# Kernel optimization log

Hardware: AMD Instinct MI355X
Metric: run time of the kernel (lower is better)

## Reference

```python
import jax, jax.numpy as jnp
import numpy as np

B, S, D = 2, 2048, 768
H = 12
DH = D // H
EPS = 1e-12


def setup_inputs() -> dict:
    key = jax.random.key(0)
    ks = jax.random.split(key, 16)
    s = 0.02
    return {
        "hidden_states": jax.random.normal(ks[0], (B, S, D), jnp.float32),
        "attention_mask": jnp.zeros((B, 1, 1, S), jnp.float32),
        "position_bias": jax.random.normal(ks[1], (1, H, S, S), jnp.float32),
        "q_w": jax.random.normal(ks[2], (D, D), jnp.float32) * s,
        "q_b": jnp.zeros((D,), jnp.float32),
        "k_w": jax.random.normal(ks[3], (D, D), jnp.float32) * s,
        "k_b": jnp.zeros((D,), jnp.float32),
        "v_w": jax.random.normal(ks[4], (D, D), jnp.float32) * s,
        "v_b": jnp.zeros((D,), jnp.float32),
        "o_w": jax.random.normal(ks[5], (D, D), jnp.float32) * s,
        "o_b": jnp.zeros((D,), jnp.float32),
        "ln_w": jnp.ones((D,), jnp.float32),
        "ln_b": jnp.zeros((D,), jnp.float32),
    }


def _split_heads(x):
    # [B, S, D] -> [B, H, S, DH]
    b, s, _ = x.shape
    return x.reshape(b, s, H, DH).transpose(0, 2, 1, 3)


def reference(hidden_states, attention_mask, position_bias,
              q_w, q_b, k_w, k_b, v_w, v_b, o_w, o_b, ln_w, ln_b):
    # nn.Linear: y = x @ W.T + b (W stored [out, in])
    q = _split_heads(hidden_states @ q_w.T + q_b)
    k = _split_heads(hidden_states @ k_w.T + k_b)
    v = _split_heads(hidden_states @ v_w.T + v_b)

    scale = 1.0 / jnp.sqrt(jnp.asarray(DH, hidden_states.dtype))
    scores = jnp.einsum('bhqd,bhkd->bhqk', q, k) * scale
    scores = scores + position_bias + attention_mask
    probs = jax.nn.softmax(scores, axis=-1)

    c = jnp.einsum('bhqk,bhkd->bhqd', probs, v)
    c = c.transpose(0, 2, 1, 3).reshape(hidden_states.shape[0], -1, D)
    o = c @ o_w.T + o_b

    # residual + LayerNorm (dropout is identity at eval)
    x = o + hidden_states
    mu = jnp.mean(x, axis=-1, keepdims=True)
    var = jnp.mean(jnp.square(x - mu), axis=-1, keepdims=True)
    out = (x - mu) * jax.lax.rsqrt(var + EPS) * ln_w + ln_b
    return out
```

## Files before the change

### kernel.cpp

```cpp
#include <hip/hip_runtime.h>
#include <math.h>

typedef unsigned short u16;
typedef float f32x4 __attribute__((ext_vector_type(4)));
typedef __bf16 bf16x8 __attribute__((ext_vector_type(8)));

#define B_ 2
#define S_ 2048
#define D_ 768
#define H_ 12
#define DH_ 64

__device__ __forceinline__ u16 f2bf(float x) {
  union { float f; unsigned u; } v; v.f = x;
  unsigned r = v.u + 0x7fffu + ((v.u >> 16) & 1u);
  return (u16)(r >> 16);
}

__device__ __forceinline__ f32x4 zero4() { f32x4 z = {0.f, 0.f, 0.f, 0.f}; return z; }

__device__ __forceinline__ f32x4 mfma16(bf16x8 a, bf16x8 b, f32x4 c) {
  return __builtin_amdgcn_mfma_f32_16x16x32_bf16(a, b, c, 0, 0, 0);
}

__device__ __forceinline__ void gload_lds16(const void* g, void* l) {
  __builtin_amdgcn_global_load_lds((const __attribute__((address_space(1))) void*)g,
                                   (__attribute__((address_space(3))) void*)l, 16, 0, 0);
}

__global__ void cvt_kernel(const float* __restrict__ hid, const float* __restrict__ qw,
                           const float* __restrict__ kw, const float* __restrict__ vw,
                           const float* __restrict__ ow, u16* __restrict__ Hb,
                           u16* __restrict__ Wb) {
  const int NH = B_ * S_ * D_;
  const int NW = D_ * D_;
  const int T4 = (NH + 4 * NW) >> 2;
  int stride = gridDim.x * blockDim.x;
  for (int i = blockIdx.x * blockDim.x + threadIdx.x; i < T4; i += stride) {
    int e = i << 2;
    const float* src; u16* dst;
    if (e < NH) { src = hid + e; dst = Hb + e; }
    else {
      int o = e - NH;
      int m = o / NW, oo = o - m * NW;
      src = (m == 0 ? qw : m == 1 ? kw : m == 2 ? vw : ow) + oo;
      dst = Wb + o;
    }
    f32x4 v = *(const f32x4*)src;
    uint2 o2;
    o2.x = (unsigned)f2bf(v[0]) | ((unsigned)f2bf(v[1]) << 16);
    o2.y = (unsigned)f2bf(v[2]) | ((unsigned)f2bf(v[3]) << 16);
    *(uint2*)dst = o2;
  }
}

#define BM 128
#define BN 128
#define BK 64

__global__ __launch_bounds__(256) void gemm_kernel(
    const u16* __restrict__ A, const u16* __restrict__ W,
    const float* __restrict__ bq, const float* __restrict__ bk, const float* __restrict__ bv,
    u16* __restrict__ Qb, u16* __restrict__ Kb, u16* __restrict__ Vtmp,
    float* __restrict__ Of, const float* __restrict__ bO, int mode)
{
  __shared__ __align__(16) u16 As[BM * BK];
  __shared__ __align__(16) u16 Bs[BN * BK];
  int t = threadIdx.x;
  int lane = t & 63, w = t >> 6;
  int wr = w >> 1, wc = w & 1;
  int l15 = lane & 15, l4 = lane >> 4;
  int m0 = blockIdx.y * BM, n0 = blockIdx.x * BN;

  f32x4 acc[4][4];
#pragma unroll
  for (int i = 0; i < 4; ++i)
#pragma unroll
    for (int j = 0; j < 4; ++j) acc[i][j] = zero4();

  const int K = D_;
  for (int k0 = 0; k0 < K; k0 += BK) {
    __syncthreads();
#pragma unroll
    for (int p = 0; p < 4; ++p) {
      int seg = p * 4 + w;
      int bd = seg * 64 + lane;
      int row = bd >> 3;
      int slot = (bd & 7) ^ (row & 7);
      gload_lds16(A + (size_t)(m0 + row) * K + k0 + slot * 8, (char*)As + seg * 1024);
      gload_lds16(W + (size_t)(n0 + row) * K + k0 + slot * 8, (char*)Bs + seg * 1024);
    }
    __syncthreads();
#pragma unroll
    for (int kk = 0; kk < 2; ++kk) {
      bf16x8 af[4], bfr[4];
#pragma unroll
      for (int i = 0; i < 4; ++i) {
        int ra = wr * 64 + i * 16 + l15;
        af[i] = *(const bf16x8*)((const char*)As + ra * 128 +
                                 ((kk * 64 + (l4 << 4)) ^ ((ra & 7) << 4)));
        int rb = wc * 64 + i * 16 + l15;
        bfr[i] = *(const bf16x8*)((const char*)Bs + rb * 128 +
                                  ((kk * 64 + (l4 << 4)) ^ ((rb & 7) << 4)));
      }
#pragma unroll
      for (int i = 0; i < 4; ++i)
#pragma unroll
        for (int j = 0; j < 4; ++j)
          acc[i][j] = mfma16(af[i], bfr[j], acc[i][j]);
    }
  }

  if (mode == 0) {
    int mat = n0 / D_;
    int ncol0 = (n0 - mat * D_) + wc * 64;
    const float* bias = (mat == 0) ? bq : (mat == 1 ? bk : bv);
    u16* outp = (mat == 0) ? Qb : (mat == 1 ? Kb : Vtmp);
    float scale = (mat == 0) ? 0.125f : 1.0f;
    int h = ncol0 >> 6;
#pragma unroll
    for (int j = 0; j < 4; ++j) {
      int d = j * 16 + l15;
      float bvv = bias[ncol0 + d];
#pragma unroll
      for (int i = 0; i < 4; ++i) {
#pragma unroll
        for (int r = 0; r < 4; ++r) {
          int m = m0 + wr * 64 + i * 16 + (l4 << 2) + r;
          int bb = m >> 11, ss = m & 2047;
          float val = (acc[i][j][r] + bvv) * scale;
          outp[(((size_t)bb * H_ + h) * S_ + ss) * DH_ + d] = f2bf(val);
        }
      }
    }
  } else {
#pragma unroll
    for (int j = 0; j < 4; ++j) {
      int n = n0 + wc * 64 + j * 16 + l15;
      float bvv = bO[n];
#pragma unroll
      for (int i = 0; i < 4; ++i) {
#pragma unroll
        for (int r = 0; r < 4; ++r) {
          int m = m0 + wr * 64 + i * 16 + (l4 << 2) + r;
          Of[(size_t)m * D_ + n] = acc[i][j][r] + bvv;
        }
      }
    }
  }
}

__global__ __launch_bounds__(256) void vtrans_kernel(const u16* __restrict__ V,
                                                     u16* __restrict__ Vt) {
  __shared__ __align__(16) u16 tile[64 * 64];
  int t = threadIdx.x;
  int s0 = blockIdx.x * 64;
  int bh = blockIdx.y;
  const u16* src = V + ((size_t)bh * S_ + s0) * DH_;
#pragma unroll
  for (int p = 0; p < 2; ++p) {
    int bd = t + p * 256;
    int row = bd >> 3, slot = bd & 7;
    uint4 v = *(const uint4*)(src + row * 64 + slot * 8);
    *(uint4*)((char*)tile + row * 128 + ((slot ^ (row & 7)) << 4)) = v;
  }
  __syncthreads();
  int d = t >> 2, sc = (t & 3) * 16;
  u16* dst = Vt + ((size_t)bh * DH_ + d) * S_ + s0 + sc;
  int colB = d * 2;
#pragma unroll
  for (int half = 0; half < 2; ++half) {
    u16 tmp[8] __attribute__((aligned(16)));
#pragma unroll
    for (int j = 0; j < 8; ++j) {
      int s = sc + half * 8 + j;
      tmp[j] = *(const u16*)((const char*)tile + s * 128 +
                             (((colB >> 4) ^ (s & 7)) << 4) + (colB & 15));
    }
    *(uint4*)(dst + half * 8) = *(const uint4*)tmp;
  }
}

__global__ __launch_bounds__(512, 6) void attn_kernel(
    const u16* __restrict__ Qb, const u16* __restrict__ Kb, const u16* __restrict__ Vt,
    const float* __restrict__ bias, const float* __restrict__ mask, u16* __restrict__ Cb)
{
  __shared__ __align__(16) u16 Ks[2][64 * 64];
  __shared__ __align__(16) u16 Vs[2][64 * 64];
  __shared__ __align__(16) char upool[17408];
  u16 (*Ps)[16][72] = (u16 (*)[16][72])upool;
  float (*Osh)[16][66] = (float (*)[16][66])upool;
  float (*Lsh)[2][16] = (float (*)[2][16])(upool + 16896);

  int t = threadIdx.x, lane = t & 63, w = t >> 6;
  int qg = w & 3, kg = w >> 2;
  int q0 = blockIdx.x * 64, h = blockIdx.y, b = blockIdx.z;
  size_t bh = (size_t)b * H_ + h;
  const u16* Qp = Qb + (bh * S_ + q0) * DH_;
  const u16* Kp = Kb + bh * S_ * DH_;
  const u16* Vp = Vt + bh * DH_ * S_;
  const float* biasp = bias + ((size_t)h * S_ + q0) * S_;
  const float* maskp = mask + (size_t)b * S_;
  int l15 = lane & 15, l4 = lane >> 4;
  int kc0 = kg * 32;

  const float* brp0 = biasp + (size_t)(qg * 16 + (l4 << 2) + 0) * S_ + kc0 + l15;
  const float* brp1 = brp0 + S_;
  const float* brp2 = brp1 + S_;
  const float* brp3 = brp2 + S_;
  const float* mkp = maskp + kc0 + l15;

  bf16x8 qf0, qf1;
  {
    const u16* qrow = Qp + (qg * 16 + l15) * DH_;
    qf0 = *(const bf16x8*)(qrow + l4 * 8);
    qf1 = *(const bf16x8*)(qrow + 32 + l4 * 8);
  }

  f32x4 oacc[4];
#pragma unroll
  for (int i = 0; i < 4; ++i) oacc[i] = zero4();
  float lrow[4] = {0.f, 0.f, 0.f, 0.f};

  float bc0[2], bc1[2], bc2[2], bc3[2];
  float bn0[2], bn1[2], bn2[2], bn3[2];

  {
    int row = t >> 3;
    int slot = (t & 7) ^ (row & 7);
    gload_lds16(Kp + (size_t)row * DH_ + slot * 8, (char*)Ks[0] + w * 1024);
    gload_lds16(Vp + (size_t)row * S_ + slot * 8, (char*)Vs[0] + w * 1024);
  }
#pragma unroll
  for (int kf = 0; kf < 2; ++kf) {
    float mk = mkp[kf * 16];
    bc0[kf] = brp0[kf * 16] + mk;
    bc1[kf] = brp1[kf * 16] + mk;
    bc2[kf] = brp2[kf * 16] + mk;
    bc3[kf] = brp3[kf * 16] + mk;
  }
  __syncthreads();

  int cur = 0;
  for (int kt = 0; kt < S_ / 64; ++kt) {
    int k0 = kt * 64;
    if (kt + 1 < S_ / 64) {
      int k0n = k0 + 64;
      int row = t >> 3;
      int slot = (t & 7) ^ (row & 7);
      gload_lds16(Kp + (size_t)(k0n + row) * DH_ + slot * 8, (char*)Ks[cur ^ 1] + w * 1024);
      gload_lds16(Vp + (size_t)row * S_ + k0n + slot * 8, (char*)Vs[cur ^ 1] + w * 1024);
#pragma unroll
      for (int kf = 0; kf < 2; ++kf) {
        float mk = mkp[k0n + kf * 16];
        bn0[kf] = brp0[k0n + kf * 16] + mk;
        bn1[kf] = brp1[k0n + kf * 16] + mk;
        bn2[kf] = brp2[k0n + kf * 16] + mk;
        bn3[kf] = brp3[k0n + kf * 16] + mk;
      }
    }

    const u16* Kc = Ks[cur];
    const u16* Vc = Vs[cur];

    f32x4 sf[2];
#pragma unroll
    for (int kf = 0; kf < 2; ++kf) {
      int row = kc0 + kf * 16 + l15;
      bf16x8 kb0 = *(const bf16x8*)((const char*)Kc + row * 128 +
                                    ((l4 << 4) ^ ((row & 7) << 4)));
      bf16x8 kb1 = *(const bf16x8*)((const char*)Kc + row * 128 +
                                    ((64 + (l4 << 4)) ^ ((row & 7) << 4)));
      f32x4 s0 = zero4();
      s0 = mfma16(qf0, kb0, s0);
      s0 = mfma16(qf1, kb1, s0);
      sf[kf] = s0;
    }

#pragma unroll
    for (int kf = 0; kf < 2; ++kf) {
      float p0 = __expf(sf[kf][0] + bc0[kf]);
      float p1 = __expf(sf[kf][1] + bc1[kf]);
      float p2 = __expf(sf[kf][2] + bc2[kf]);
      float p3 = __expf(sf[kf][3] + bc3[kf]);
      sf[kf][0] = p0; sf[kf][1] = p1; sf[kf][2] = p2; sf[kf][3] = p3;
      lrow[0] += p0; lrow[1] += p1; lrow[2] += p2; lrow[3] += p3;
    }

#pragma unroll
    for (int r = 0; r < 4; ++r)
#pragma unroll
      for (int kf = 0; kf < 2; ++kf)
        Ps[qg][(l4 << 2) + r][kc0 + kf * 16 + l15] = f2bf(sf[kf][r]);

    bf16x8 pa = *(const bf16x8*)&Ps[qg][l15][kc0 + l4 * 8];

#pragma unroll
    for (int df = 0; df < 4; ++df) {
      int row = df * 16 + l15;
      bf16x8 vb = *(const bf16x8*)((const char*)Vc + row * 128 +
                                   ((kg * 64 + (l4 << 4)) ^ ((row & 7) << 4)));
      oacc[df] = mfma16(pa, vb, oacc[df]);
    }

    __syncthreads();
    cur ^= 1;
#pragma unroll
    for (int kf = 0; kf < 2; ++kf) {
      bc0[kf] = bn0[kf]; bc1[kf] = bn1[kf];
      bc2[kf] = bn2[kf]; bc3[kf] = bn3[kf];
    }
  }

#pragma unroll
  for (int r = 0; r < 4; ++r) {
#pragma unroll
    for (int o = 1; o < 16; o <<= 1) lrow[r] += __shfl_xor(lrow[r], o, 64);
  }
  if (l15 == 0) {
#pragma unroll
    for (int r = 0; r < 4; ++r) Lsh[qg][kg][(l4 << 2) + r] = lrow[r];
  }
  if (kg == 1) {
#pragma unroll
    for (int r = 0; r < 4; ++r)
#pragma unroll
      for (int df = 0; df < 4; ++df)
        Osh[qg][(l4 << 2) + r][df * 16 + l15] = oacc[df][r];
  }
  __syncthreads();
  if (kg == 0) {
#pragma unroll
    for (int r = 0; r < 4; ++r) {
      int rr = (l4 << 2) + r;
      float inv = 1.0f / (Lsh[qg][0][rr] + Lsh[qg][1][rr]);
      int q = q0 + qg * 16 + rr;
      size_t base = ((size_t)b * S_ + q) * D_ + h * DH_ + l15;
#pragma unroll
      for (int df = 0; df < 4; ++df)
        Cb[base + df * 16] = f2bf((oacc[df][r] + Osh[qg][rr][df * 16 + l15]) * inv);
    }
  }
}

__global__ __launch_bounds__(192) void ln_kernel(const float* __restrict__ O,
                                                 const float* __restrict__ hid,
                                                 const float* __restrict__ lw,
                                                 const float* __restrict__ lb,
                                                 float* __restrict__ out) {
  int row = blockIdx.x, t = threadIdx.x;
  size_t base = (size_t)row * D_;
  f32x4 x = *(const f32x4*)(O + base + t * 4);
  f32x4 hh = *(const f32x4*)(hid + base + t * 4);
  x = x + hh;
  float s = x[0] + x[1] + x[2] + x[3];
  float s2 = x[0] * x[0] + x[1] * x[1] + x[2] * x[2] + x[3] * x[3];
#pragma unroll
  for (int o = 1; o < 64; o <<= 1) {
    s += __shfl_xor(s, o, 64);
    s2 += __shfl_xor(s2, o, 64);
  }
  __shared__ float rs[3], rs2[3];
  int w = t >> 6, lane = t & 63;
  if (lane == 0) { rs[w] = s; rs2[w] = s2; }
  __syncthreads();
  s = rs[0] + rs[1] + rs[2];
  s2 = rs2[0] + rs2[1] + rs2[2];
  float mu = s * (1.0f / 768.0f);
  float var = s2 * (1.0f / 768.0f) - mu * mu;
  float rstd = rsqrtf(var + 1e-12f);
  f32x4 w4 = *(const f32x4*)(lw + t * 4);
  f32x4 b4 = *(const f32x4*)(lb + t * 4);
  f32x4 y = (x - mu) * rstd * w4 + b4;
  *(f32x4*)(out + base + t * 4) = y;
}

extern "C" void kernel_launch(void* const* d_in, const int* in_sizes, int n_in,
                              void* d_out, int out_size, void* d_ws, size_t ws_size,
                              hipStream_t stream) {
  const float* hid  = (const float*)d_in[0];
  const float* mask = (const float*)d_in[1];
  const float* bias = (const float*)d_in[2];
  const float* qw = (const float*)d_in[3];
  const float* qb = (const float*)d_in[4];
  const float* kw = (const float*)d_in[5];
  const float* kb = (const float*)d_in[6];
  const float* vw = (const float*)d_in[7];
  const float* vb = (const float*)d_in[8];
  const float* ow = (const float*)d_in[9];
  const float* ob = (const float*)d_in[10];
  const float* lnw = (const float*)d_in[11];
  const float* lnb = (const float*)d_in[12];

  char* ws = (char*)d_ws;
  const size_t NHB = (size_t)B_ * S_ * D_ * 2;
  const size_t NWB = (size_t)4 * D_ * D_ * 2;
  const size_t NQB = (size_t)B_ * H_ * S_ * DH_ * 2;
  u16* Hb = (u16*)ws;
  u16* Wb = (u16*)(ws + NHB);
  u16* Qb = (u16*)(ws + NHB + NWB);
  u16* Kb = (u16*)(ws + NHB + NWB + NQB);
  u16* Vt = (u16*)(ws + NHB + NWB + 2 * NQB);
  u16* Cb = (u16*)(ws + NHB + NWB + 3 * NQB);
  float* Of = (float*)(ws + NHB + NWB + 4 * NQB);
  u16* Vtmp = (u16*)Of;

  cvt_kernel<<<2048, 256, 0, stream>>>(hid, qw, kw, vw, ow, Hb, Wb);

  gemm_kernel<<<dim3(18, 32), 256, 0, stream>>>(
      Hb, Wb, qb, kb, vb, Qb, Kb, Vtmp, nullptr, nullptr, 0);

  vtrans_kernel<<<dim3(S_ / 64, B_ * H_), 256, 0, stream>>>(Vtmp, Vt);

  attn_kernel<<<dim3(S_ / 64, H_, B_), 512, 0, stream>>>(Qb, Kb, Vt, bias, mask, Cb);

  gemm_kernel<<<dim3(6, 32), 256, 0, stream>>>(
      Cb, Wb + (size_t)3 * D_ * D_, nullptr, nullptr, nullptr,
      nullptr, nullptr, nullptr, Of, ob, 1);

  ln_kernel<<<B_ * S_, 192, 0, stream>>>(Of, hid, lnw, lnb, (float*)d_out);
}
```

Measured before the change: 149.8 us.

## Replace async LDS loads with register-staged two-tile-ahead prefetch pipeline

```diff
diff --git a/kernel.cpp b/kernel.cpp
--- a/kernel.cpp
+++ b/kernel.cpp
@@ -181,7 +181,7 @@
   }
 }
 
-__global__ __launch_bounds__(512, 6) void attn_kernel(
+__global__ __launch_bounds__(512, 4) void attn_kernel(
     const u16* __restrict__ Qb, const u16* __restrict__ Kb, const u16* __restrict__ Vt,
     const float* __restrict__ bias, const float* __restrict__ mask, u16* __restrict__ Cb)
 {
@@ -210,6 +210,11 @@
   const float* brp3 = brp2 + S_;
   const float* mkp = maskp + kc0 + l15;
 
+  int srow = t >> 3, sslot = t & 7;
+  const u16* gK = Kp + (size_t)srow * DH_ + sslot * 8;
+  const u16* gV = Vp + (size_t)srow * S_ + sslot * 8;
+  int lofs = srow * 128 + ((sslot ^ (srow & 7)) << 4);
+
   bf16x8 qf0, qf1;
   {
     const u16* qrow = Qp + (qg * 16 + l15) * DH_;
@@ -222,94 +227,143 @@
   for (int i = 0; i < 4; ++i) oacc[i] = zero4();
   float lrow[4] = {0.f, 0.f, 0.f, 0.f};
 
-  float bc0[2], bc1[2], bc2[2], bc3[2];
-  float bn0[2], bn1[2], bn2[2], bn3[2];
-
-  {
-    int row = t >> 3;
-    int slot = (t & 7) ^ (row & 7);
-    gload_lds16(Kp + (size_t)row * DH_ + slot * 8, (char*)Ks[0] + w * 1024);
-    gload_lds16(Vp + (size_t)row * S_ + slot * 8, (char*)Vs[0] + w * 1024);
-  }
+  uint4 stKe, stVe, stKo, stVo;
+  float bA0[2], bA1[2], bA2[2], bA3[2], mA[2];
+  float bB0[2], bB1[2], bB2[2], bB3[2], mB[2];
+
+  stKe = *(const uint4*)gK;
+  stVe = *(const uint4*)gV;
 #pragma unroll
   for (int kf = 0; kf < 2; ++kf) {
-    float mk = mkp[kf * 16];
-    bc0[kf] = brp0[kf * 16] + mk;
-    bc1[kf] = brp1[kf * 16] + mk;
-    bc2[kf] = brp2[kf * 16] + mk;
-    bc3[kf] = brp3[kf * 16] + mk;
-  }
+    bA0[kf] = brp0[kf * 16];        bA1[kf] = brp1[kf * 16];
+    bA2[kf] = brp2[kf * 16];        bA3[kf] = brp3[kf * 16];
+    mA[kf]  = mkp[kf * 16];
+    bB0[kf] = brp0[64 + kf * 16];   bB1[kf] = brp1[64 + kf * 16];
+    bB2[kf] = brp2[64 + kf * 16];   bB3[kf] = brp3[64 + kf * 16];
+    mB[kf]  = mkp[64 + kf * 16];
+  }
+  *(uint4*)((char*)Ks[0] + lofs) = stKe;
+  *(uint4*)((char*)Vs[0] + lofs) = stVe;
+  stKo = *(const uint4*)(gK + 4096);
+  stVo = *(const uint4*)(gV + 64);
+  stKe = *(const uint4*)(gK + 2 * 4096);
+  stVe = *(const uint4*)(gV + 2 * 64);
   __syncthreads();
 
-  int cur = 0;
-  for (int kt = 0; kt < S_ / 64; ++kt) {
-    int k0 = kt * 64;
-    if (kt + 1 < S_ / 64) {
-      int k0n = k0 + 64;
-      int row = t >> 3;
-      int slot = (t & 7) ^ (row & 7);
-      gload_lds16(Kp + (size_t)(k0n + row) * DH_ + slot * 8, (char*)Ks[cur ^ 1] + w * 1024);
-      gload_lds16(Vp + (size_t)row * S_ + k0n + slot * 8, (char*)Vs[cur ^ 1] + w * 1024);
+  for (int kt = 0; kt < 32; kt += 2) {
+    *(uint4*)((char*)Ks[1] + lofs) = stKo;
+    *(uint4*)((char*)Vs[1] + lofs) = stVo;
+    if (kt + 3 < 32) {
+      stKo = *(const uint4*)(gK + (size_t)(kt + 3) * 4096);
+      stVo = *(const uint4*)(gV + (size_t)(kt + 3) * 64);
+    }
+    {
+      const u16* Kc = Ks[0];
+      const u16* Vc = Vs[0];
+      f32x4 sf[2];
 #pragma unroll
       for (int kf = 0; kf < 2; ++kf) {
-        float mk = mkp[k0n + kf * 16];
-        bn0[kf] = brp0[k0n + kf * 16] + mk;
-        bn1[kf] = brp1[k0n + kf * 16] + mk;
-        bn2[kf] = brp2[k0n + kf * 16] + mk;
-        bn3[kf] = brp3[k0n + kf * 16] + mk;
-      }
-    }
-
-    const u16* Kc = Ks[cur];
-    const u16* Vc = Vs[cur];
-
-    f32x4 sf[2];
-#pragma unroll
-    for (int kf = 0; kf < 2; ++kf) {
-      int row = kc0 + kf * 16 + l15;
-      bf16x8 kb0 = *(const bf16x8*)((const char*)Kc + row * 128 +
-                                    ((l4 << 4) ^ ((row & 7) << 4)));
-      bf16x8 kb1 = *(const bf16x8*)((const char*)Kc + row * 128 +
-                                    ((64 + (l4 << 4)) ^ ((row & 7) << 4)));
-      f32x4 s0 = zero4();
-      s0 = mfma16(qf0, kb0, s0);
-      s0 = mfma16(qf1, kb1, s0);
-      sf[kf] = s0;
-    }
-
-#pragma unroll
-    for (int kf = 0; kf < 2; ++kf) {
-      float p0 = __expf(sf[kf][0] + bc0[kf]);
-      float p1 = __expf(sf[kf][1] + bc1[kf]);
-      float p2 = __expf(sf[kf][2] + bc2[kf]);
-      float p3 = __expf(sf[kf][3] + bc3[kf]);
-      sf[kf][0] = p0; sf[kf][1] = p1; sf[kf][2] = p2; sf[kf][3] = p3;
-      lrow[0] += p0; lrow[1] += p1; lrow[2] += p2; lrow[3] += p3;
-    }
-
-#pragma unroll
-    for (int r = 0; r < 4; ++r)
-#pragma unroll
-      for (int kf = 0; kf < 2; ++kf)
-        Ps[qg][(l4 << 2) + r][kc0 + kf * 16 + l15] = f2bf(sf[kf][r]);
-
-    bf16x8 pa = *(const bf16x8*)&Ps[qg][l15][kc0 + l4 * 8];
-
-#pragma unroll
-    for (int df = 0; df < 4; ++df) {
-      int row = df * 16 + l15;
-      bf16x8 vb = *(const bf16x8*)((const char*)Vc + row * 128 +
-                                   ((kg * 64 + (l4 << 4)) ^ ((row & 7) << 4)));
-      oacc[df] = mfma16(pa, vb, oacc[df]);
-    }
-
+        int row = kc0 + kf * 16 + l15;
+        bf16x8 kb0 = *(const bf16x8*)((const char*)Kc + row * 128 +
+                                      ((l4 << 4) ^ ((row & 7) << 4)));
+        bf16x8 kb1 = *(const bf16x8*)((const char*)Kc + row * 128 +
+                                      ((64 + (l4 << 4)) ^ ((row & 7) << 4)));
+        f32x4 s0 = zero4();
+        s0 = mfma16(qf0, kb0, s0);
+        s0 = mfma16(qf1, kb1, s0);
+        sf[kf] = s0;
+      }
+#pragma unroll
+      for (int kf = 0; kf < 2; ++kf) {
+        float p0 = __expf(sf[kf][0] + bA0[kf] + mA[kf]);
+        float p1 = __expf(sf[kf][1] + bA1[kf] + mA[kf]);
+        float p2 = __expf(sf[kf][2] + bA2[kf] + mA[kf]);
+        float p3 = __expf(sf[kf][3] + bA3[kf] + mA[kf]);
+        sf[kf][0] = p0; sf[kf][1] = p1; sf[kf][2] = p2; sf[kf][3] = p3;
+        lrow[0] += p0; lrow[1] += p1; lrow[2] += p2; lrow[3] += p3;
+      }
+      if (kt + 2 < 32) {
+        int kb2 = (kt + 2) * 64;
+#pragma unroll
+        for (int kf = 0; kf < 2; ++kf) {
+          bA0[kf] = brp0[kb2 + kf * 16]; bA1[kf] = brp1[kb2 + kf * 16];
+          bA2[kf] = brp2[kb2 + kf * 16]; bA3[kf] = brp3[kb2 + kf * 16];
+          mA[kf]  = mkp[kb2 + kf * 16];
+        }
+      }
+#pragma unroll
+      for (int r = 0; r < 4; ++r)
+#pragma unroll
+        for (int kf = 0; kf < 2; ++kf)
+          Ps[qg][(l4 << 2) + r][kc0 + kf * 16 + l15] = f2bf(sf[kf][r]);
+      bf16x8 pa = *(const bf16x8*)&Ps[qg][l15][kc0 + l4 * 8];
+#pragma unroll
+      for (int df = 0; df < 4; ++df) {
+        int row = df * 16 + l15;
+        bf16x8 vb = *(const bf16x8*)((const char*)Vc + row * 128 +
+                                     ((kg * 64 + (l4 << 4)) ^ ((row & 7) << 4)));
+        oacc[df] = mfma16(pa, vb, oacc[df]);
+      }
+    }
     __syncthreads();
-    cur ^= 1;
-#pragma unroll
-    for (int kf = 0; kf < 2; ++kf) {
-      bc0[kf] = bn0[kf]; bc1[kf] = bn1[kf];
-      bc2[kf] = bn2[kf]; bc3[kf] = bn3[kf];
-    }
+
+    if (kt + 2 < 32) {
+      *(uint4*)((char*)Ks[0] + lofs) = stKe;
+      *(uint4*)((char*)Vs[0] + lofs) = stVe;
+      if (kt + 4 < 32) {
+        stKe = *(const uint4*)(gK + (size_t)(kt + 4) * 4096);
+        stVe = *(const uint4*)(gV + (size_t)(kt + 4) * 64);
+      }
+    }
+    {
+      const u16* Kc = Ks[1];
+      const u16* Vc = Vs[1];
+      f32x4 sf[2];
+#pragma unroll
+      for (int kf = 0; kf < 2; ++kf) {
+        int row = kc0 + kf * 16 + l15;
+        bf16x8 kb0 = *(const bf16x8*)((const char*)Kc + row * 128 +
+                                      ((l4 << 4) ^ ((row & 7) << 4)));
+        bf16x8 kb1 = *(const bf16x8*)((const char*)Kc + row * 128 +
+                                      ((64 + (l4 << 4)) ^ ((row & 7) << 4)));
+        f32x4 s0 = zero4();
+        s0 = mfma16(qf0, kb0, s0);
+        s0 = mfma16(qf1, kb1, s0);
+        sf[kf] = s0;
+      }
+#pragma unroll
+      for (int kf = 0; kf < 2; ++kf) {
+        float p0 = __expf(sf[kf][0] + bB0[kf] + mB[kf]);
+        float p1 = __expf(sf[kf][1] + bB1[kf] + mB[kf]);
+        float p2 = __expf(sf[kf][2] + bB2[kf] + mB[kf]);
+        float p3 = __expf(sf[kf][3] + bB3[kf] + mB[kf]);
+        sf[kf][0] = p0; sf[kf][1] = p1; sf[kf][2] = p2; sf[kf][3] = p3;
+        lrow[0] += p0; lrow[1] += p1; lrow[2] += p2; lrow[3] += p3;
+      }
+      if (kt + 3 < 32) {
+        int kb3 = (kt + 3) * 64;
+#pragma unroll
+        for (int kf = 0; kf < 2; ++kf) {
+          bB0[kf] = brp0[kb3 + kf * 16]; bB1[kf] = brp1[kb3 + kf * 16];
+          bB2[kf] = brp2[kb3 + kf * 16]; bB3[kf] = brp3[kb3 + kf * 16];
+          mB[kf]  = mkp[kb3 + kf * 16];
+        }
+      }
+#pragma unroll
+      for (int r = 0; r < 4; ++r)
+#pragma unroll
+        for (int kf = 0; kf < 2; ++kf)
+          Ps[qg][(l4 << 2) + r][kc0 + kf * 16 + l15] = f2bf(sf[kf][r]);
+      bf16x8 pa = *(const bf16x8*)&Ps[qg][l15][kc0 + l4 * 8];
+#pragma unroll
+      for (int df = 0; df < 4; ++df) {
+        int row = df * 16 + l15;
+        bf16x8 vb = *(const bf16x8*)((const char*)Vc + row * 128 +
+                                     ((kg * 64 + (l4 << 4)) ^ ((row & 7) << 4)));
+        oacc[df] = mfma16(pa, vb, oacc[df]);
+      }
+    }
+    __syncthreads();
   }
 
 #pragma unroll
```

Measured after the change: 157.5 us. 1.05x slower.
